# Kernel optimization log

Measured on AMD Instinct MI355X. Metric: run time of the kernel, lower is better.

The kernel has to match this reference:

```python
import jax, jax.numpy as jnp
import numpy as np

V = 65536      # vocab_size_v
H = 512        # hidden_size
M = 16         # max word length (m)
N = 8192       # number of words in the ragged batch
IH = H // 4    # char embedding dim / LSTM input size
HH = H // 2    # LSTM hidden size per direction


def setup_inputs() -> dict:
    key = jax.random.key(0)
    ks = jax.random.split(key, 16)
    word_ids = jax.random.randint(ks[0], (N,), 0, V, dtype=jnp.int32)
    is_oov = jax.random.randint(ks[1], (N,), 0, 2, dtype=jnp.int32)
    char_ids = jax.random.randint(ks[2], (N, M), 0, 256, dtype=jnp.int32)
    char_lens = jax.random.randint(ks[3], (N,), 1, M + 1, dtype=jnp.int32)
    lstm_scale = 1.0 / np.sqrt(HH)
    return {
        "word_ids": word_ids,
        "is_oov": is_oov,
        "char_ids": char_ids,
        "char_lens": char_lens,
        "word_emb": jax.random.normal(ks[4], (V, H), jnp.float32) * 0.02,
        "char_emb": jax.random.normal(ks[5], (256, IH), jnp.float32) * 0.02,
        "w_ih_f": jax.random.uniform(ks[6], (4 * HH, IH), jnp.float32, -lstm_scale, lstm_scale),
        "w_hh_f": jax.random.uniform(ks[7], (4 * HH, HH), jnp.float32, -lstm_scale, lstm_scale),
        "b_ih_f": jax.random.uniform(ks[8], (4 * HH,), jnp.float32, -lstm_scale, lstm_scale),
        "b_hh_f": jax.random.uniform(ks[9], (4 * HH,), jnp.float32, -lstm_scale, lstm_scale),
        "w_ih_b": jax.random.uniform(ks[10], (4 * HH, IH), jnp.float32, -lstm_scale, lstm_scale),
        "w_hh_b": jax.random.uniform(ks[11], (4 * HH, HH), jnp.float32, -lstm_scale, lstm_scale),
        "b_ih_b": jax.random.uniform(ks[12], (4 * HH,), jnp.float32, -lstm_scale, lstm_scale),
        "b_hh_b": jax.random.uniform(ks[13], (4 * HH,), jnp.float32, -lstm_scale, lstm_scale),
        "proj_w": jax.random.normal(ks[14], (H, H), jnp.float32) * 0.02,
        "proj_b": jax.random.normal(ks[15], (H,), jnp.float32) * 0.02,
    }


def _lstm_final_hidden(x, lens, w_ih, w_hh, b_ih, b_hh):
    """Batched variable-length LSTM; returns final hidden state h_T per sequence.

    x: [N, M, IH], lens: [N]. Carry is frozen once t >= len (emulating per-word
    batch-size-1 LSTM calls on unpadded sequences). PyTorch gate order i,f,g,o.
    """
    n = x.shape[0]
    gx = jnp.einsum("nmi,gi->nmg", x, w_ih) + b_ih + b_hh        # [N, M, 4HH]
    mask = (jnp.arange(M)[None, :] < lens[:, None])[..., None]    # [N, M, 1]

    def step(carry, inp):
        h, c = carry
        g_t, m_t = inp                                            # [N,4HH], [N,1]
        g = g_t + h @ w_hh.T
        i, f, gg, o = jnp.split(g, 4, axis=-1)
        i = jax.nn.sigmoid(i)
        f = jax.nn.sigmoid(f)
        gg = jnp.tanh(gg)
        o = jax.nn.sigmoid(o)
        c_new = f * c + i * gg
        h_new = o * jnp.tanh(c_new)
        h = jnp.where(m_t, h_new, h)
        c = jnp.where(m_t, c_new, c)
        return (h, c), None

    h0 = jnp.zeros((n, HH), x.dtype)
    c0 = jnp.zeros((n, HH), x.dtype)
    (h, _), _ = jax.lax.scan(step, (h0, c0),
                             (gx.transpose(1, 0, 2), mask.transpose(1, 0, 2)))
    return h  # [N, HH]


def reference(word_ids, is_oov, char_ids, char_lens,
              word_emb, char_emb,
              w_ih_f, w_hh_f, b_ih_f, b_hh_f,
              w_ih_b, w_hh_b, b_ih_b, b_hh_b,
              proj_w, proj_b):
    # Char-level path (computed for all words, selected only where OOV).
    x = char_emb[char_ids]                                        # [N, M, IH]
    h_fwd = _lstm_final_hidden(x, char_lens, w_ih_f, w_hh_f, b_ih_f, b_hh_f)
    # Backward direction: reverse each sequence within its true length.
    rev_idx = jnp.clip(char_lens[:, None] - 1 - jnp.arange(M)[None, :], 0, M - 1)
    x_rev = jnp.take_along_axis(x, rev_idx[..., None], axis=1)    # [N, M, IH]
    h_bwd = _lstm_final_hidden(x_rev, char_lens, w_ih_b, w_hh_b, b_ih_b, b_hh_b)
    char_word_embed = jnp.concatenate([h_fwd, h_bwd], axis=-1)    # [N, H]

    vocab_embed = word_emb[word_ids]                              # [N, H]
    sel = jnp.where(is_oov[:, None] > 0, char_word_embed, vocab_embed)
    return sel @ proj_w.T + proj_b                                # [N, H]
```

## Files before the change

### kernel.cpp

```cpp
#include <hip/hip_runtime.h>
#include <math.h>

#define VOCAB   65536
#define HDIM    512
#define MLEN    16
#define NWORDS  8192
#define IHDIM   128
#define HHDIM   256

#define TMW 32
#define TW  16

#define B_WHH 0u
#define B_GXC 1048576u
#define B_PT  3145728u
#define B_CHE 4194304u
#define B_INT 12582912u

typedef _Float16 f16x8 __attribute__((ext_vector_type(8)));
typedef float    f32x4 __attribute__((ext_vector_type(4)));
union U4H8 { uint4 u; f16x8 h; };

__device__ __forceinline__ unsigned packh2(float lo, float hi) {
    union { _Float16 h[2]; unsigned u; } v;
    v.h[0] = (_Float16)lo; v.h[1] = (_Float16)hi;
    return v.u;
}

__device__ __forceinline__ float sigf(float x)  { return 1.0f / (1.0f + __expf(-x)); }
__device__ __forceinline__ float tanh_f(float x){ return 1.0f - 2.0f / (__expf(2.0f * x) + 1.0f); }

__device__ __forceinline__ void load_lds_128(const void* g, void* l) {
    __builtin_amdgcn_global_load_lds((const __attribute__((address_space(1))) unsigned*)g,
                                     (__attribute__((address_space(3))) unsigned*)l, 16, 0, 0);
}

__global__ void prep_k(const float* __restrict__ whhf, const float* __restrict__ whhb,
                       const float* __restrict__ projw, char* __restrict__ wsb) {
    int i = blockIdx.x * blockDim.x + threadIdx.x;
    if (i < 65536) {
        int dir = i >> 15, r = i & 32767, kt = r >> 12, r2 = r & 4095, ntg = r2 >> 6, lane = r2 & 63;
        const float* whh = dir ? whhb : whhf;
        int n  = ntg * 16 + (lane & 15);
        int k0 = kt * 32 + (lane >> 4) * 8;
        unsigned q[4];
        #pragma unroll
        for (int jj = 0; jj < 4; ++jj)
            q[jj] = packh2(whh[n * HHDIM + k0 + 2 * jj], whh[n * HHDIM + k0 + 2 * jj + 1]);
        ((uint4*)(wsb + B_WHH))[i] = make_uint4(q[0], q[1], q[2], q[3]);
    }
    if (i < 262144) {
        int k4 = i >> 11, r = i & 2047, j = r >> 2, kk = r & 3;
        ((float*)(wsb + B_PT))[i] = projw[j * HDIM + k4 * 4 + kk];
    }
}

__global__ void gxc_k(const float* __restrict__ wihf, const float* __restrict__ wihb,
                      const float* __restrict__ bihf, const float* __restrict__ bhhf,
                      const float* __restrict__ bihb, const float* __restrict__ bhhb,
                      const float* __restrict__ chemb, char* __restrict__ wsb) {
    const int dir = blockIdx.x >> 8, cid = blockIdx.x & 255;
    __shared__ __align__(16) float emb[IHDIM];
    if (threadIdx.x < IHDIM) emb[threadIdx.x] = chemb[cid * IHDIM + threadIdx.x];
    __syncthreads();
    const float* wih = dir ? wihb : wihf;
    const float* bih = dir ? bihb : bihf;
    const float* bhh = dir ? bhhb : bhhf;
    float* gxc = (float*)(wsb + B_GXC) + (size_t)dir * 262144 + (size_t)cid * 1024;
    #pragma unroll
    for (int p = 0; p < 4; ++p) {
        int n = threadIdx.x + p * 256;
        float acc = bih[n] + bhh[n];
        const float4* w4 = (const float4*)(wih + n * IHDIM);
        const float4* e4 = (const float4*)emb;
        #pragma unroll 8
        for (int k4 = 0; k4 < 32; ++k4) {
            float4 w = w4[k4], e = e4[k4];
            acc = fmaf(w.x, e.x, fmaf(w.y, e.y, fmaf(w.z, e.z, fmaf(w.w, e.w, acc))));
        }
        gxc[n] = acc;
    }
}

__global__ void count_k(const int* __restrict__ is_oov, const int* __restrict__ lens,
                        int* __restrict__ ip) {
    int n = blockIdx.x * blockDim.x + threadIdx.x;
    if (n < NWORDS && is_oov[n] > 0) atomicAdd(&ip[lens[n] - 1], 1);
}

__global__ void prefix_k(int* __restrict__ ip) {
    if (threadIdx.x == 0) {
        int total = 0;
        for (int b = 15; b >= 0; --b) { ip[16 + b] = total; ip[32 + b] = total; total += ip[b]; }
        ip[48] = total;
    }
}

__global__ void scatter_k(const int* __restrict__ is_oov, const int* __restrict__ lens,
                          int* __restrict__ ip) {
    int n = blockIdx.x * blockDim.x + threadIdx.x;
    if (n < NWORDS && is_oov[n] > 0) {
        int pos = atomicAdd(&ip[32 + lens[n] - 1], 1);
        ip[64 + pos] = n;
    }
}

__global__ __launch_bounds__(512, 2)
void lstm_k(const int* __restrict__ char_ids, const int* __restrict__ lens,
            const char* __restrict__ wsb, const int* __restrict__ ip) {
    const int dir = blockIdx.y;
    const int tid = threadIdx.x;
    const int total = ip[48];
    const int w0 = blockIdx.x * TMW;
    if (w0 >= total) return;
    const int wcount = min(TMW, total - w0);
    const int* sorted = ip + 64;

    __shared__ int n_s[TMW], len_s[TMW];
    __shared__ int cid_s[MLEN][TMW];
    __shared__ __align__(16) _Float16 Zh[TMW][264];
    __shared__ __align__(16) uint4 wbuf[8][2][512];

    if (tid < TMW) {
        int idx = w0 + min(tid, wcount - 1);
        n_s[tid] = sorted[idx];
        len_s[tid] = (tid < wcount) ? lens[sorted[idx]] : 0;
    }
    for (int i = tid; i < TMW * 132; i += 512) ((unsigned*)Zh)[i] = 0u;
    __syncthreads();
    {
        int m = tid >> 4, t = tid & 15;
        int L = len_s[m];
        int pos = dir ? max(L - 1 - t, 0) : t;
        cid_s[t][m] = char_ids[n_s[m] * MLEN + pos];
    }

    const int wv = tid >> 6, lane = tid & 63, col = lane & 15, quad = lane >> 4;
    int lenr[2][4];
    #pragma unroll
    for (int mt = 0; mt < 2; ++mt)
        #pragma unroll
        for (int r = 0; r < 4; ++r) lenr[mt][r] = len_s[mt * 16 + quad * 4 + r];
    const int maxlen = len_s[0];

    const uint4* wpg = (const uint4*)(wsb + B_WHH) + (size_t)dir * 32768;
    const float* gxc = (const float*)(wsb + B_GXC) + (size_t)dir * 262144;

    float cst[2][2][4];
    #pragma unroll
    for (int c = 0; c < 2; ++c)
        #pragma unroll
        for (int mt = 0; mt < 2; ++mt)
            #pragma unroll
            for (int r = 0; r < 4; ++r) cst[c][mt][r] = 0.0f;

    auto stage = [&](int kt, int buf) {
        #pragma unroll
        for (int gc = 0; gc < 8; ++gc) {
            int ntg = (gc >> 1) * 16 + wv * 2 + (gc & 1);
            load_lds_128(wpg + (kt * 4096 + ntg * 64 + lane), &wbuf[wv][buf][gc * 64]);
        }
    };
    stage(0, 0);
    __syncthreads();

    for (int t = 0; t < maxlen; ++t) {
        int cids[2][4];
        #pragma unroll
        for (int mt = 0; mt < 2; ++mt)
            #pragma unroll
            for (int r = 0; r < 4; ++r) cids[mt][r] = cid_s[t][mt * 16 + quad * 4 + r];

        f32x4 acc[4][2][2];
        #pragma unroll
        for (int g = 0; g < 4; ++g)
            #pragma unroll
            for (int c = 0; c < 2; ++c) {
                const int nn = g * 256 + wv * 32 + c * 16 + col;
                #pragma unroll
                for (int mt = 0; mt < 2; ++mt) {
                    f32x4 a;
                    #pragma unroll
                    for (int r = 0; r < 4; ++r) a[r] = gxc[cids[mt][r] * 1024 + nn];
                    acc[g][c][mt] = a;
                }
            }

        #pragma unroll
        for (int kt = 0; kt < 8; ++kt) {
            const int buf = kt & 1;
            stage((kt + 1) & 7, buf ^ 1);
            __builtin_amdgcn_s_waitcnt(0x0F78);
            f16x8 af0 = *(const f16x8*)&Zh[col][kt * 32 + quad * 8];
            f16x8 af1 = *(const f16x8*)&Zh[16 + col][kt * 32 + quad * 8];
            #pragma unroll
            for (int g = 0; g < 4; ++g)
                #pragma unroll
                for (int c = 0; c < 2; ++c) {
                    U4H8 b; b.u = wbuf[wv][buf][(g * 2 + c) * 64 + lane];
                    acc[g][c][0] = __builtin_amdgcn_mfma_f32_16x16x32_f16(af0, b.h, acc[g][c][0], 0, 0, 0);
                    acc[g][c][1] = __builtin_amdgcn_mfma_f32_16x16x32_f16(af1, b.h, acc[g][c][1], 0, 0, 0);
                }
        }
        __syncthreads();

        #pragma unroll
        for (int mt = 0; mt < 2; ++mt)
            #pragma unroll
            for (int r = 0; r < 4; ++r) {
                if (t < lenr[mt][r]) {
                    const int m = mt * 16 + quad * 4 + r;
                    #pragma unroll
                    for (int c = 0; c < 2; ++c) {
                        float i_ = sigf(acc[0][c][mt][r]);
                        float f_ = sigf(acc[1][c][mt][r]);
                        float g_ = tanh_f(acc[2][c][mt][r]);
                        float o_ = sigf(acc[3][c][mt][r]);
                        float cn = f_ * cst[c][mt][r] + i_ * g_;
                        cst[c][mt][r] = cn;
                        Zh[m][wv * 32 + c * 16 + col] = (_Float16)(o_ * tanh_f(cn));
                    }
                }
            }
        __syncthreads();
    }

    unsigned short* cheh = (unsigned short*)(wsb + B_CHE);
    for (int i = tid; i < TMW * HHDIM; i += 512) {
        int m = i >> 8, u = i & 255;
        if (m < wcount) {
            union { _Float16 h; unsigned short s; } v; v.h = Zh[m][u];
            __builtin_nontemporal_store(v.s, cheh + (size_t)n_s[m] * HDIM + dir * HHDIM + u);
        }
    }
}

__global__ __launch_bounds__(256, 2)
void proj_k(const int* __restrict__ word_ids, const int* __restrict__ is_oov,
            const float* __restrict__ word_emb, const char* __restrict__ wsb,
            const float* __restrict__ proj_b, float* __restrict__ out) {
    const int tid = threadIdx.x;
    const int n0 = blockIdx.x * TW;
    __shared__ __align__(16) float4 sel[TW][128];

    for (int f = tid; f < TW * 128; f += 256) {
        int w = f >> 7, k4 = f & 127;
        int n = n0 + w;
        float4 v;
        if (is_oov[n] > 0) {
            const ushort4* src = (const ushort4*)(wsb + B_CHE) + (size_t)n * 128;
            ushort4 hv = src[k4];
            union { unsigned short s; _Float16 h; } a, b, c, d;
            a.s = hv.x; b.s = hv.y; c.s = hv.z; d.s = hv.w;
            v = make_float4((float)a.h, (float)b.h, (float)c.h, (float)d.h);
        } else {
            v = ((const float4*)(word_emb + (size_t)word_ids[n] * HDIM))[k4];
        }
        sel[w][k4] = v;
    }
    __syncthreads();

    const float pb0 = proj_b[tid];
    const float pb1 = proj_b[tid + 256];
    float acc0[TW], acc1[TW];
    #pragma unroll
    for (int w = 0; w < TW; ++w) { acc0[w] = pb0; acc1[w] = pb1; }

    const float4* pT4 = (const float4*)(wsb + B_PT);
    for (int k4 = 0; k4 < 128; ++k4) {
        const float4 p0 = pT4[k4 * 512 + tid];
        const float4 p1 = pT4[k4 * 512 + tid + 256];
        #pragma unroll
        for (int w = 0; w < TW; ++w) {
            const float4 z = sel[w][k4];
            acc0[w] = fmaf(p0.x, z.x, fmaf(p0.y, z.y, fmaf(p0.z, z.z, fmaf(p0.w, z.w, acc0[w]))));
            acc1[w] = fmaf(p1.x, z.x, fmaf(p1.y, z.y, fmaf(p1.z, z.z, fmaf(p1.w, z.w, acc1[w]))));
        }
    }
    #pragma unroll
    for (int w = 0; w < TW; ++w) {
        __builtin_nontemporal_store(acc0[w], &out[(size_t)(n0 + w) * HDIM + tid]);
        __builtin_nontemporal_store(acc1[w], &out[(size_t)(n0 + w) * HDIM + tid + 256]);
    }
}

extern "C" void kernel_launch(void* const* d_in, const int* in_sizes, int n_in,
                              void* d_out, int out_size, void* d_ws, size_t ws_size,
                              hipStream_t stream) {
    const int*   word_ids  = (const int*)d_in[0];
    const int*   is_oov    = (const int*)d_in[1];
    const int*   char_ids  = (const int*)d_in[2];
    const int*   char_lens = (const int*)d_in[3];
    const float* word_emb  = (const float*)d_in[4];
    const float* char_emb  = (const float*)d_in[5];
    const float* w_ih_f    = (const float*)d_in[6];
    const float* w_hh_f    = (const float*)d_in[7];
    const float* b_ih_f    = (const float*)d_in[8];
    const float* b_hh_f    = (const float*)d_in[9];
    const float* w_ih_b    = (const float*)d_in[10];
    const float* w_hh_b    = (const float*)d_in[11];
    const float* b_ih_b    = (const float*)d_in[12];
    const float* b_hh_b    = (const float*)d_in[13];
    const float* proj_w    = (const float*)d_in[14];
    const float* proj_b    = (const float*)d_in[15];
    float* out = (float*)d_out;
    char*  wsb = (char*)d_ws;
    int*   ip  = (int*)(wsb + B_INT);

    hipMemsetAsync(ip, 0, 256, stream);
    prep_k<<<1024, 256, 0, stream>>>(w_hh_f, w_hh_b, proj_w, wsb);
    gxc_k<<<512, 256, 0, stream>>>(w_ih_f, w_ih_b, b_ih_f, b_hh_f, b_ih_b, b_hh_b, char_emb, wsb);
    count_k<<<NWORDS / 256, 256, 0, stream>>>(is_oov, char_lens, ip);
    prefix_k<<<1, 64, 0, stream>>>(ip);
    scatter_k<<<NWORDS / 256, 256, 0, stream>>>(is_oov, char_lens, ip);
    lstm_k<<<dim3(NWORDS / TMW, 2), 512, 0, stream>>>(char_ids, char_lens, wsb, ip);
    proj_k<<<NWORDS / TW, 256, 0, stream>>>(word_ids, is_oov, word_emb, wsb, proj_b, out);
}
```

Baseline: 521.8 us.

## Use fp16 MFMA for projection and pack gate-input table in fp16 lane layout

The projection GEMM moves from scalar fp32 FMAs to fp16 MFMA 16x16x32, with proj_w pre-packed into MFMA B-fragment order and 32 words per 512-thread block. The per-character input-gate table is stored as fp16 in a per-lane layout, so each LSTM step fetches one uint4 per row instead of many scattered fp32 loads. Both changes cut memory traffic and instruction count. In exchange, the projection inputs and gate inputs lose precision by being rounded to fp16.

```diff
diff --git a/kernel.cpp b/kernel.cpp
--- a/kernel.cpp
+++ b/kernel.cpp
@@ -9,17 +9,18 @@
 #define HHDIM   256
 
 #define TMW 32
-#define TW  16
+#define TP  32
 
 #define B_WHH 0u
-#define B_GXC 1048576u
-#define B_PT  3145728u
-#define B_CHE 4194304u
-#define B_INT 12582912u
+#define B_GX2 1048576u
+#define B_PBF 5242880u
+#define B_PBB 5767168u
+#define B_CHE 5769216u
+#define B_INT 14157824u
 
 typedef _Float16 f16x8 __attribute__((ext_vector_type(8)));
 typedef float    f32x4 __attribute__((ext_vector_type(4)));
-union U4H8 { uint4 u; f16x8 h; };
+union U4H8 { uint4 u; f16x8 h; _Float16 e[8]; };
 
 __device__ __forceinline__ unsigned packh2(float lo, float hi) {
     union { _Float16 h[2]; unsigned u; } v;
@@ -36,7 +37,8 @@
 }
 
 __global__ void prep_k(const float* __restrict__ whhf, const float* __restrict__ whhb,
-                       const float* __restrict__ projw, char* __restrict__ wsb) {
+                       const float* __restrict__ projw, const float* __restrict__ projb,
+                       char* __restrict__ wsb) {
     int i = blockIdx.x * blockDim.x + threadIdx.x;
     if (i < 65536) {
         int dir = i >> 15, r = i & 32767, kt = r >> 12, r2 = r & 4095, ntg = r2 >> 6, lane = r2 & 63;
@@ -49,10 +51,17 @@
             q[jj] = packh2(whh[n * HHDIM + k0 + 2 * jj], whh[n * HHDIM + k0 + 2 * jj + 1]);
         ((uint4*)(wsb + B_WHH))[i] = make_uint4(q[0], q[1], q[2], q[3]);
     }
-    if (i < 262144) {
-        int k4 = i >> 11, r = i & 2047, j = r >> 2, kk = r & 3;
-        ((float*)(wsb + B_PT))[i] = projw[j * HDIM + k4 * 4 + kk];
-    }
+    if (i < 32768) {
+        int kt = i >> 11, r = i & 2047, nt = r >> 6, lane = r & 63;
+        int j  = nt * 16 + (lane & 15);
+        int k0 = kt * 32 + (lane >> 4) * 8;
+        unsigned q[4];
+        #pragma unroll
+        for (int jj = 0; jj < 4; ++jj)
+            q[jj] = packh2(projw[j * HDIM + k0 + 2 * jj], projw[j * HDIM + k0 + 2 * jj + 1]);
+        ((uint4*)(wsb + B_PBF))[i] = make_uint4(q[0], q[1], q[2], q[3]);
+    }
+    if (i < 512) ((float*)(wsb + B_PBB))[i] = projb[i];
 }
 
 __global__ void gxc_k(const float* __restrict__ wihf, const float* __restrict__ wihb,
@@ -61,12 +70,12 @@
                       const float* __restrict__ chemb, char* __restrict__ wsb) {
     const int dir = blockIdx.x >> 8, cid = blockIdx.x & 255;
     __shared__ __align__(16) float emb[IHDIM];
+    __shared__ float gxl[1024];
     if (threadIdx.x < IHDIM) emb[threadIdx.x] = chemb[cid * IHDIM + threadIdx.x];
     __syncthreads();
     const float* wih = dir ? wihb : wihf;
     const float* bih = dir ? bihb : bihf;
     const float* bhh = dir ? bhhb : bhhf;
-    float* gxc = (float*)(wsb + B_GXC) + (size_t)dir * 262144 + (size_t)cid * 1024;
     #pragma unroll
     for (int p = 0; p < 4; ++p) {
         int n = threadIdx.x + p * 256;
@@ -78,7 +87,21 @@
             float4 w = w4[k4], e = e4[k4];
             acc = fmaf(w.x, e.x, fmaf(w.y, e.y, fmaf(w.z, e.z, fmaf(w.w, e.w, acc))));
         }
-        gxc[n] = acc;
+        gxl[n] = acc;
+    }
+    __syncthreads();
+    uint4* outp = (uint4*)(wsb + B_GX2) + (size_t)(dir * 256 + cid) * 512;
+    #pragma unroll
+    for (int s = 0; s < 2; ++s) {
+        int tid2 = threadIdx.x + s * 256;
+        int wv = tid2 >> 6, col = tid2 & 15;
+        U4H8 v;
+        #pragma unroll
+        for (int g = 0; g < 4; ++g)
+            #pragma unroll
+            for (int c = 0; c < 2; ++c)
+                v.e[g * 2 + c] = (_Float16)gxl[g * 256 + wv * 32 + c * 16 + col];
+        outp[tid2] = v.u;
     }
 }
 
@@ -144,7 +167,7 @@
     const int maxlen = len_s[0];
 
     const uint4* wpg = (const uint4*)(wsb + B_WHH) + (size_t)dir * 32768;
-    const float* gxc = (const float*)(wsb + B_GXC) + (size_t)dir * 262144;
+    const uint4* gx2 = (const uint4*)(wsb + B_GX2) + (size_t)dir * 131072;
 
     float cst[2][2][4];
     #pragma unroll
@@ -165,26 +188,25 @@
     __syncthreads();
 
     for (int t = 0; t < maxlen; ++t) {
-        int cids[2][4];
+        U4H8 gq[2][4];
         #pragma unroll
         for (int mt = 0; mt < 2; ++mt)
             #pragma unroll
-            for (int r = 0; r < 4; ++r) cids[mt][r] = cid_s[t][mt * 16 + quad * 4 + r];
+            for (int r = 0; r < 4; ++r)
+                gq[mt][r].u = gx2[(size_t)cid_s[t][mt * 16 + quad * 4 + r] * 512 + tid];
 
         f32x4 acc[4][2][2];
         #pragma unroll
         for (int g = 0; g < 4; ++g)
             #pragma unroll
-            for (int c = 0; c < 2; ++c) {
-                const int nn = g * 256 + wv * 32 + c * 16 + col;
+            for (int c = 0; c < 2; ++c)
                 #pragma unroll
                 for (int mt = 0; mt < 2; ++mt) {
                     f32x4 a;
                     #pragma unroll
-                    for (int r = 0; r < 4; ++r) a[r] = gxc[cids[mt][r] * 1024 + nn];
+                    for (int r = 0; r < 4; ++r) a[r] = (float)gq[mt][r].e[g * 2 + c];
                     acc[g][c][mt] = a;
                 }
-            }
 
         #pragma unroll
         for (int kt = 0; kt < 8; ++kt) {
@@ -235,53 +257,62 @@
     }
 }
 
-__global__ __launch_bounds__(256, 2)
+__global__ __launch_bounds__(512, 2)
 void proj_k(const int* __restrict__ word_ids, const int* __restrict__ is_oov,
             const float* __restrict__ word_emb, const char* __restrict__ wsb,
-            const float* __restrict__ proj_b, float* __restrict__ out) {
+            float* __restrict__ out) {
     const int tid = threadIdx.x;
-    const int n0 = blockIdx.x * TW;
-    __shared__ __align__(16) float4 sel[TW][128];
-
-    for (int f = tid; f < TW * 128; f += 256) {
-        int w = f >> 7, k4 = f & 127;
+    const int n0 = blockIdx.x * TP;
+    __shared__ __align__(16) _Float16 Zp[TP][520];
+
+    for (int f = tid; f < TP * 128; f += 512) {
+        int w = f >> 7, s4 = f & 127;
         int n = n0 + w;
-        float4 v;
         if (is_oov[n] > 0) {
-            const ushort4* src = (const ushort4*)(wsb + B_CHE) + (size_t)n * 128;
-            ushort4 hv = src[k4];
-            union { unsigned short s; _Float16 h; } a, b, c, d;
-            a.s = hv.x; b.s = hv.y; c.s = hv.z; d.s = hv.w;
-            v = make_float4((float)a.h, (float)b.h, (float)c.h, (float)d.h);
+            ushort4 hv = ((const ushort4*)((const unsigned short*)(wsb + B_CHE) + (size_t)n * HDIM))[s4];
+            *(ushort4*)&Zp[w][s4 * 4] = hv;
         } else {
-            v = ((const float4*)(word_emb + (size_t)word_ids[n] * HDIM))[k4];
-        }
-        sel[w][k4] = v;
-    }
-    __syncthreads();
-
-    const float pb0 = proj_b[tid];
-    const float pb1 = proj_b[tid + 256];
-    float acc0[TW], acc1[TW];
-    #pragma unroll
-    for (int w = 0; w < TW; ++w) { acc0[w] = pb0; acc1[w] = pb1; }
-
-    const float4* pT4 = (const float4*)(wsb + B_PT);
-    for (int k4 = 0; k4 < 128; ++k4) {
-        const float4 p0 = pT4[k4 * 512 + tid];
-        const float4 p1 = pT4[k4 * 512 + tid + 256];
-        #pragma unroll
-        for (int w = 0; w < TW; ++w) {
-            const float4 z = sel[w][k4];
-            acc0[w] = fmaf(p0.x, z.x, fmaf(p0.y, z.y, fmaf(p0.z, z.z, fmaf(p0.w, z.w, acc0[w]))));
-            acc1[w] = fmaf(p1.x, z.x, fmaf(p1.y, z.y, fmaf(p1.z, z.z, fmaf(p1.w, z.w, acc1[w]))));
-        }
-    }
-    #pragma unroll
-    for (int w = 0; w < TW; ++w) {
-        __builtin_nontemporal_store(acc0[w], &out[(size_t)(n0 + w) * HDIM + tid]);
-        __builtin_nontemporal_store(acc1[w], &out[(size_t)(n0 + w) * HDIM + tid + 256]);
-    }
+            float4 v = ((const float4*)(word_emb + (size_t)word_ids[n] * HDIM))[s4];
+            Zp[w][s4 * 4 + 0] = (_Float16)v.x;
+            Zp[w][s4 * 4 + 1] = (_Float16)v.y;
+            Zp[w][s4 * 4 + 2] = (_Float16)v.z;
+            Zp[w][s4 * 4 + 3] = (_Float16)v.w;
+        }
+    }
+    __syncthreads();
+
+    const int wv = tid >> 6, lane = tid & 63, col = lane & 15, quad = lane >> 4;
+    const float* pbb = (const float*)(wsb + B_PBB);
+    f32x4 acc[4][2];
+    #pragma unroll
+    for (int c = 0; c < 4; ++c) {
+        float b = pbb[wv * 64 + c * 16 + col];
+        acc[c][0] = (f32x4){b, b, b, b};
+        acc[c][1] = (f32x4){b, b, b, b};
+    }
+
+    const uint4* pbf = (const uint4*)(wsb + B_PBF);
+    #pragma unroll
+    for (int kt = 0; kt < 16; ++kt) {
+        f16x8 af0 = *(const f16x8*)&Zp[col][kt * 32 + quad * 8];
+        f16x8 af1 = *(const f16x8*)&Zp[16 + col][kt * 32 + quad * 8];
+        #pragma unroll
+        for (int c = 0; c < 4; ++c) {
+            U4H8 b; b.u = pbf[(size_t)kt * 2048 + (wv * 4 + c) * 64 + lane];
+            acc[c][0] = __builtin_amdgcn_mfma_f32_16x16x32_f16(af0, b.h, acc[c][0], 0, 0, 0);
+            acc[c][1] = __builtin_amdgcn_mfma_f32_16x16x32_f16(af1, b.h, acc[c][1], 0, 0, 0);
+        }
+    }
+
+    #pragma unroll
+    for (int mt = 0; mt < 2; ++mt)
+        #pragma unroll
+        for (int r = 0; r < 4; ++r) {
+            const size_t m = n0 + mt * 16 + quad * 4 + r;
+            #pragma unroll
+            for (int c = 0; c < 4; ++c)
+                __builtin_nontemporal_store(acc[c][mt][r], &out[m * HDIM + wv * 64 + c * 16 + col]);
+        }
 }
 
 extern "C" void kernel_launch(void* const* d_in, const int* in_sizes, int n_in,
@@ -308,11 +339,11 @@
     int*   ip  = (int*)(wsb + B_INT);
 
     hipMemsetAsync(ip, 0, 256, stream);
-    prep_k<<<1024, 256, 0, stream>>>(w_hh_f, w_hh_b, proj_w, wsb);
+    prep_k<<<256, 256, 0, stream>>>(w_hh_f, w_hh_b, proj_w, proj_b, wsb);
     gxc_k<<<512, 256, 0, stream>>>(w_ih_f, w_ih_b, b_ih_f, b_hh_f, b_ih_b, b_hh_b, char_emb, wsb);
     count_k<<<NWORDS / 256, 256, 0, stream>>>(is_oov, char_lens, ip);
     prefix_k<<<1, 64, 0, stream>>>(ip);
     scatter_k<<<NWORDS / 256, 256, 0, stream>>>(is_oov, char_lens, ip);
     lstm_k<<<dim3(NWORDS / TMW, 2), 512, 0, stream>>>(char_ids, char_lens, wsb, ip);
-    proj_k<<<NWORDS / TW, 256, 0, stream>>>(word_ids, is_oov, word_emb, wsb, proj_b, out);
-}
+    proj_k<<<NWORDS / TP, 512, 0, stream>>>(word_ids, is_oov, word_emb, wsb, out);
+}
```

New measurement: 474.3 us. 1.1x faster.
